# Kernel tuning notes

Measured on AMD Instinct MI355X. Metric: run time of the kernel, lower is better.

## Reference

```python
import jax, jax.numpy as jnp
import numpy as np

CHUNK = 64  # _HYMBA_SCAN_CHUNK default
HEAD_DIM = 128
STATE_DIM = 128


def setup_inputs() -> dict:
    key = jax.random.key(0)
    ks = jax.random.split(key, 6)
    B, T = 8, 8192
    x = jax.random.normal(ks[0], (B, T, HEAD_DIM), dtype=jnp.float32)
    log_A = jax.random.normal(ks[1], (STATE_DIM,), dtype=jnp.float32) * 0.5
    # torch Linear weights are (out_features, in_features); kaiming-uniform-ish init
    lim = 1.0 / np.sqrt(HEAD_DIM)
    W_B = jax.random.uniform(ks[2], (STATE_DIM, HEAD_DIM), jnp.float32, -lim, lim)
    W_C = jax.random.uniform(ks[3], (STATE_DIM, HEAD_DIM), jnp.float32, -lim, lim)
    W_dt = jax.random.uniform(ks[4], (STATE_DIM, HEAD_DIM), jnp.float32, -lim, lim)
    b_dt = jnp.full((STATE_DIM,), -4.0, dtype=jnp.float32)
    lim_o = 1.0 / np.sqrt(STATE_DIM)
    W_out = jax.random.uniform(ks[5], (HEAD_DIM, STATE_DIM), jnp.float32, -lim_o, lim_o)
    return {"x": x, "log_A": log_A, "W_B": W_B, "W_C": W_C,
            "W_dt": W_dt, "b_dt": b_dt, "W_out": W_out}


def _scan_chunks(log_a, u, chunk_size=CHUNK):
    # log_a, u: (B, T, S) fp32; exact chunk-parallel diagonal recurrence
    B, T, S = u.shape
    nc = T // chunk_size
    la = log_a.reshape(B, nc, chunk_size, S).transpose(1, 0, 2, 3)  # (nc,B,ck,S)
    uu = u.reshape(B, nc, chunk_size, S).transpose(1, 0, 2, 3)

    def step(h0, inp):
        la_c, u_c = inp                                   # (B, ck, S)
        log_p = jnp.clip(jnp.cumsum(la_c, axis=1), -30.0, 0.0)
        p = jnp.exp(log_p)
        h = p * jnp.cumsum(u_c * jnp.exp(-log_p), axis=1) + p * h0[:, None, :]
        return h[:, -1, :], h

    h0 = jnp.zeros((B, S), dtype=jnp.float32)
    _, h_chunks = jax.lax.scan(step, h0, (la, uu))        # (nc, B, ck, S)
    return h_chunks.transpose(1, 0, 2, 3).reshape(B, T, S)


def reference(x, log_A, W_B, W_C, W_dt, b_dt, W_out):
    xf = x.astype(jnp.float32)
    dt = jnp.minimum(jax.nn.softplus(jnp.einsum('btd,sd->bts', xf, W_dt) + b_dt), 1.0)
    A = -jnp.minimum(jnp.exp(log_A.astype(jnp.float32)), 10.0)   # (S,)
    log_a = jnp.clip(dt * A[None, None, :], -0.5, 0.0)
    Bx = jnp.einsum('btd,sd->bts', xf, W_B) * dt
    C = jnp.einsum('btd,sd->bts', xf, W_C)
    h = _scan_chunks(log_a, Bx)                                   # (B,T,S)
    y = jnp.sum(C * h, axis=-1, keepdims=True)                    # (B,T,1)
    out = jnp.einsum('bts,ds->btd', h.astype(x.dtype), W_out)
    return out + y.astype(x.dtype) * x[..., :1]
```

## Files before the change

### kernel.cpp

```cpp
#include <hip/hip_runtime.h>
#include <hip/hip_bf16.h>

#define B_ 8
#define T_ 8192
#define D_ 128
#define S_ 128
#define CK 64
#define NC 128
#define NCHUNK (B_*NC)

typedef __attribute__((ext_vector_type(8))) __bf16 bf16x8;
typedef __attribute__((ext_vector_type(4))) float floatx4;

#define WS_WBF     0
#define WS_AVEC    32768
#define WS_PART    32896

__device__ __forceinline__ unsigned short f2bf(float f) {
  __hip_bfloat16 b = __float2bfloat16(f);
  return *(unsigned short*)&b;
}

__device__ __forceinline__ float softplus1(float z) {
  float sp = fmaxf(z, 0.0f) + __logf(1.0f + __expf(-fabsf(z)));
  return fminf(sp, 1.0f);
}

__device__ __forceinline__ unsigned long long part_load(const unsigned long long* p) {
  return __hip_atomic_load(p, __ATOMIC_RELAXED, __HIP_MEMORY_SCOPE_AGENT);
}
__device__ __forceinline__ void part_store(unsigned long long* p, unsigned long long v) {
  __hip_atomic_store(p, v, __ATOMIC_RELAXED, __HIP_MEMORY_SCOPE_AGENT);
}

__global__ __launch_bounds__(256) void k0_prep(
    const float* __restrict__ Wdt, const float* __restrict__ WB,
    const float* __restrict__ WC,  const float* __restrict__ Wout,
    const float* __restrict__ logA, float* __restrict__ ws) {
  unsigned short* wb = (unsigned short*)(ws + WS_WBF);
  const float* srcs[4] = {Wdt, WB, WC, Wout};
  int gid = blockIdx.x * 256 + threadIdx.x;
#pragma unroll
  for (int r = 0; r < 2; ++r) {
    int fid = gid * 2 + r;
    int lane = fid & 63;
    int kk   = (fid >> 6) & 3;
    int nt   = (fid >> 8) & 7;
    int m    = fid >> 11;
    int c = lane & 15, g = lane >> 4;
    const float* src = srcs[m] + (16 * nt + c) * 128 + 32 * kk + 8 * g;
    float4 v0 = *(const float4*)src;
    float4 v1 = *(const float4*)(src + 4);
    unsigned short o[8];
    o[0] = f2bf(v0.x); o[1] = f2bf(v0.y); o[2] = f2bf(v0.z); o[3] = f2bf(v0.w);
    o[4] = f2bf(v1.x); o[5] = f2bf(v1.y); o[6] = f2bf(v1.z); o[7] = f2bf(v1.w);
    *(ushort4*)&wb[fid * 8]     = *(ushort4*)&o[0];
    *(ushort4*)&wb[fid * 8 + 4] = *(ushort4*)&o[4];
  }
  unsigned long long* part = (unsigned long long*)(ws + WS_PART);
#pragma unroll
  for (int i = 0; i < 32; ++i)
    part[gid + 4096 * i] = 0ull;
  if (blockIdx.x == 0 && threadIdx.x < 128)
    ws[WS_AVEC + threadIdx.x] = -fminf(expf(logA[threadIdx.x]), 10.0f);
}

#define WFRAG(mat, nt, kk) \
  (*(const bf16x8*)&wb[(((((mat) * 8 + (nt)) * 4) + (kk)) * 64 + lane) * 8])

__global__ __launch_bounds__(256, 2) void k_main(
    const float* __restrict__ x, const float* __restrict__ bdt,
    float* __restrict__ out, float* __restrict__ ws) {
  __shared__ __align__(16) unsigned short xb[64 * 136];
  __shared__ float wlsP[4 * 128];
  __shared__ float wlsH[4 * 128];
  __shared__ float h0buf[128];
  __shared__ float yx[64];

  const int tid  = threadIdx.x;
  const int bc   = blockIdx.x;
  const int b    = bc & 7;
  const int cidx = bc >> 3;
  const long chunk_t0 = (long)b * T_ + (long)cidx * CK;
  const int w    = tid >> 6;
  const int lane = tid & 63;
  const int g    = lane >> 4;
  const int c    = lane & 15;

  float Av[8], Bd[8];
#pragma unroll
  for (int nt = 0; nt < 8; ++nt) {
    Av[nt] = ws[WS_AVEC + 16 * nt + c];
    Bd[nt] = bdt[16 * nt + c];
  }
  float x0[4];
  if (c == 0) {
#pragma unroll
    for (int i = 0; i < 4; ++i)
      x0[i] = x[(chunk_t0 + 16 * w + 4 * g + i) * D_];
  }

  const float4* x4 = (const float4*)(x + chunk_t0 * D_);
#pragma unroll
  for (int i = 0; i < 8; ++i) {
    int f4 = tid + 256 * i;
    int t  = f4 >> 5;
    int d0 = (f4 & 31) << 2;
    float4 v = x4[f4];
    ushort4 o;
    o.x = f2bf(v.x); o.y = f2bf(v.y); o.z = f2bf(v.z); o.w = f2bf(v.w);
    *(ushort4*)&xb[t * 136 + d0] = o;
  }
  __syncthreads();

  bf16x8 afr[4];
#pragma unroll
  for (int kk = 0; kk < 4; ++kk)
    afr[kk] = *(const bf16x8*)&xb[(16 * w + c) * 136 + 8 * g + 32 * kk];

  const unsigned short* wb = (const unsigned short*)(ws + WS_WBF);
  unsigned long long* part = (unsigned long long*)(ws + WS_PART);

  floatx4 dtacc[8], bacc[8];
#pragma unroll
  for (int nt = 0; nt < 8; ++nt) {
    dtacc[nt] = (floatx4){0.f, 0.f, 0.f, 0.f};
    bacc[nt]  = (floatx4){0.f, 0.f, 0.f, 0.f};
  }

  {
    bf16x8 fD[8], fB[8];
#pragma unroll
    for (int nt = 0; nt < 8; ++nt) fD[nt] = WFRAG(0, nt, 0);
#pragma unroll
    for (int nt = 0; nt < 8; ++nt) fB[nt] = WFRAG(1, nt, 0);
#pragma unroll
    for (int kk = 0; kk < 4; ++kk) {
      bf16x8 nD[8], nB[8];
      if (kk < 3) {
#pragma unroll
        for (int nt = 0; nt < 8; ++nt) nD[nt] = WFRAG(0, nt, kk + 1);
#pragma unroll
        for (int nt = 0; nt < 8; ++nt) nB[nt] = WFRAG(1, nt, kk + 1);
      }
#pragma unroll
      for (int nt = 0; nt < 8; ++nt) {
        dtacc[nt] = __builtin_amdgcn_mfma_f32_16x16x32_bf16(afr[kk], fD[nt], dtacc[nt], 0, 0, 0);
        bacc[nt]  = __builtin_amdgcn_mfma_f32_16x16x32_bf16(afr[kk], fB[nt], bacc[nt], 0, 0, 0);
      }
      if (kk < 3) {
#pragma unroll
        for (int nt = 0; nt < 8; ++nt) { fD[nt] = nD[nt]; fB[nt] = nB[nt]; }
      }
    }
  }

#pragma unroll
  for (int nt = 0; nt < 8; ++nt)
#pragma unroll
    for (int i = 0; i < 4; ++i) {
      float dt = softplus1(dtacc[nt][i] + Bd[nt]);
      float u  = bacc[nt][i] * dt;
      float la = fmaxf(fminf(dt * Av[nt], 0.0f), -0.5f);
      dtacc[nt][i] = __expf(la);
      bacc[nt][i]  = u;
    }

#pragma unroll
  for (int nt = 0; nt < 8; ++nt) {
    float P = dtacc[nt][0], H = bacc[nt][0];
#pragma unroll
    for (int i = 1; i < 4; ++i) {
      H = fmaf(H, dtacc[nt][i], bacc[nt][i]);
      P = P * dtacc[nt][i];
      dtacc[nt][i] = P;
      bacc[nt][i]  = H;
    }
  }
#pragma unroll
  for (int nt = 0; nt < 8; ++nt) {
    float P = dtacc[nt][3], H = bacc[nt][3];
    float Po = __shfl(P, (lane - 16) & 63), Ho = __shfl(H, (lane - 16) & 63);
    if (g >= 1) { H = fmaf(Ho, P, H); P = Po * P; }
    Po = __shfl(P, (lane - 32) & 63); Ho = __shfl(H, (lane - 32) & 63);
    if (g >= 2) { H = fmaf(Ho, P, H); P = Po * P; }
    float Pe = __shfl(P, (lane - 16) & 63), He = __shfl(H, (lane - 16) & 63);
    if (g == 0) { Pe = 1.0f; He = 0.0f; }
#pragma unroll
    for (int i = 0; i < 4; ++i) {
      bacc[nt][i] = fmaf(dtacc[nt][i], He, bacc[nt][i]);
      dtacc[nt][i] = dtacc[nt][i] * Pe;
    }
    if (g == 3) {
      wlsP[w * 128 + 16 * nt + c] = dtacc[nt][3];
      wlsH[w * 128 + 16 * nt + c] = bacc[nt][3];
    }
  }
  __syncthreads();

  if (tid < 128) {
    float Pt = 1.0f, Ht = 0.0f;
#pragma unroll
    for (int ww = 0; ww < 4; ++ww) {
      float Pw = wlsP[ww * 128 + tid];
      float Hw = wlsH[ww * 128 + tid];
      Ht = fmaf(Ht, Pw, Hw);
      Pt = Pt * Pw;
    }
    unsigned long long v = ((unsigned long long)__float_as_uint(Ht) << 32) |
                           (unsigned long long)__float_as_uint(Pt);
    part_store(&part[bc * 128 + tid], v);
  }

#pragma unroll
  for (int nt = 0; nt < 8; ++nt) {
    float Pe = 1.0f, He = 0.0f;
    for (int ww = 0; ww < 3; ++ww) {
      if (ww < w) {
        float Pw = wlsP[ww * 128 + 16 * nt + c];
        float Hw = wlsH[ww * 128 + 16 * nt + c];
        He = fmaf(He, Pw, Hw);
        Pe = Pe * Pw;
      }
    }
#pragma unroll
    for (int i = 0; i < 4; ++i) {
      bacc[nt][i] = fmaf(dtacc[nt][i], He, bacc[nt][i]);
      dtacc[nt][i] = dtacc[nt][i] * Pe;
    }
  }

  floatx4 cacc[8];
#pragma unroll
  for (int nt = 0; nt < 8; ++nt) cacc[nt] = (floatx4){0.f, 0.f, 0.f, 0.f};
  {
    bf16x8 fC[8];
#pragma unroll
    for (int nt = 0; nt < 8; ++nt) fC[nt] = WFRAG(2, nt, 0);
#pragma unroll
    for (int kk = 0; kk < 4; ++kk) {
      bf16x8 nC[8];
      if (kk < 3) {
#pragma unroll
        for (int nt = 0; nt < 8; ++nt) nC[nt] = WFRAG(2, nt, kk + 1);
      }
#pragma unroll
      for (int nt = 0; nt < 8; ++nt)
        cacc[nt] = __builtin_amdgcn_mfma_f32_16x16x32_bf16(afr[kk], fC[nt], cacc[nt], 0, 0, 0);
      if (kk < 3) {
#pragma unroll
        for (int nt = 0; nt < 8; ++nt) fC[nt] = nC[nt];
      }
    }
  }

  __syncthreads();

  if (tid < 128) {
    float RP = 1.0f, RH = 0.0f;
    int j = cidx - 1;
    while (j >= 0) {
      int nb = (j >= 7) ? 8 : (j + 1);
      unsigned long long v[8];
#pragma unroll
      for (int q = 0; q < 8; ++q)
        if (q < nb) v[q] = part_load(&part[(((j - q) << 3) | b) * 128 + tid]);
#pragma unroll
      for (int q = 0; q < 8; ++q) {
        if (q < nb) {
          unsigned long long vv = v[q];
          const unsigned long long* ap = &part[(((j - q) << 3) | b) * 128 + tid];
          while ((unsigned)vv == 0u) {
            __builtin_amdgcn_s_sleep(2);
            vv = part_load(ap);
          }
          float Pj = __uint_as_float((unsigned)vv);
          float Hj = __uint_as_float((unsigned)(vv >> 32));
          RH = fmaf(RP, Hj, RH);
          RP = RP * Pj;
        }
      }
      j -= nb;
    }
    h0buf[tid] = RH;
  }
  __syncthreads();

  float h0[8];
#pragma unroll
  for (int nt = 0; nt < 8; ++nt) h0[nt] = h0buf[16 * nt + c];

  float yv[4] = {0.f, 0.f, 0.f, 0.f};
  unsigned short* hT = xb;
#pragma unroll
  for (int nt = 0; nt < 8; ++nt)
#pragma unroll
    for (int i = 0; i < 4; ++i) {
      float hv = fmaf(dtacc[nt][i], h0[nt], bacc[nt][i]);
      yv[i] = fmaf(cacc[nt][i], hv, yv[i]);
      hT[(16 * w + 4 * g + i) * 136 + 16 * nt + c] = f2bf(hv);
    }
#pragma unroll
  for (int i = 0; i < 4; ++i) {
    yv[i] += __shfl_xor(yv[i], 1);
    yv[i] += __shfl_xor(yv[i], 2);
    yv[i] += __shfl_xor(yv[i], 4);
    yv[i] += __shfl_xor(yv[i], 8);
  }
  if (c == 0) {
#pragma unroll
    for (int i = 0; i < 4; ++i) yx[16 * w + 4 * g + i] = yv[i] * x0[i];
  }

  bf16x8 fO[8];
#pragma unroll
  for (int nt = 0; nt < 8; ++nt) fO[nt] = WFRAG(3, nt, 0);
  __syncthreads();

  bf16x8 hfr[4];
#pragma unroll
  for (int kk = 0; kk < 4; ++kk)
    hfr[kk] = *(const bf16x8*)&hT[(16 * w + c) * 136 + 8 * g + 32 * kk];

  floatx4 oacc[8];
#pragma unroll
  for (int nt = 0; nt < 8; ++nt) oacc[nt] = (floatx4){0.f, 0.f, 0.f, 0.f};
#pragma unroll
  for (int kk = 0; kk < 4; ++kk) {
    bf16x8 nO[8];
    if (kk < 3) {
#pragma unroll
      for (int nt = 0; nt < 8; ++nt) nO[nt] = WFRAG(3, nt, kk + 1);
    }
#pragma unroll
    for (int nt = 0; nt < 8; ++nt)
      oacc[nt] = __builtin_amdgcn_mfma_f32_16x16x32_bf16(hfr[kk], fO[nt], oacc[nt], 0, 0, 0);
    if (kk < 3) {
#pragma unroll
      for (int nt = 0; nt < 8; ++nt) fO[nt] = nO[nt];
    }
  }

#pragma unroll
  for (int nt = 0; nt < 8; ++nt)
#pragma unroll
    for (int i = 0; i < 4; ++i) {
      int row = 16 * w + 4 * g + i;
      out[(chunk_t0 + row) * D_ + 16 * nt + c] = oacc[nt][i] + yx[row];
    }
}

extern "C" void kernel_launch(void* const* d_in, const int* in_sizes, int n_in,
                              void* d_out, int out_size, void* d_ws, size_t ws_size,
                              hipStream_t stream) {
  const float* x    = (const float*)d_in[0];
  const float* logA = (const float*)d_in[1];
  const float* W_B  = (const float*)d_in[2];
  const float* W_C  = (const float*)d_in[3];
  const float* W_dt = (const float*)d_in[4];
  const float* b_dt = (const float*)d_in[5];
  const float* W_out= (const float*)d_in[6];
  float* out = (float*)d_out;
  float* ws  = (float*)d_ws;

  k0_prep<<<16, 256, 0, stream>>>(W_dt, W_B, W_C, W_out, logA, ws);
  k_main<<<NCHUNK, 256, 0, stream>>>(x, b_dt, out, ws);
}
```

Measured before the change: 134.1 us.

## Repartition waves by state columns, split decoupled lookback across half-waves

The four waves now each own 32 state columns across all 64 timesteps, instead of 16 timesteps across all 128 columns. Each wave does the full intra-chunk scan on its own, so the LDS exchange of per-wave carries and one barrier go away, and each wave loads a quarter of the weight fragments. The cross-chunk lookback is split between the two halves of each wave, which walk disjoint ranges of previous chunks, and the results are combined with a shuffle. The y reduction across waves now goes through LDS, launch bounds allow 3 blocks per CU, and the prep kernel uses more blocks with less work per thread. In exchange, A fragments are re-read from LDS per M tile, which raises LDS traffic.

```diff
diff --git a/kernel.cpp b/kernel.cpp
--- a/kernel.cpp
+++ b/kernel.cpp
@@ -40,9 +40,8 @@
   unsigned short* wb = (unsigned short*)(ws + WS_WBF);
   const float* srcs[4] = {Wdt, WB, WC, Wout};
   int gid = blockIdx.x * 256 + threadIdx.x;
-#pragma unroll
-  for (int r = 0; r < 2; ++r) {
-    int fid = gid * 2 + r;
+  {
+    int fid = gid;
     int lane = fid & 63;
     int kk   = (fid >> 6) & 3;
     int nt   = (fid >> 8) & 7;
@@ -59,8 +58,8 @@
   }
   unsigned long long* part = (unsigned long long*)(ws + WS_PART);
 #pragma unroll
-  for (int i = 0; i < 32; ++i)
-    part[gid + 4096 * i] = 0ull;
+  for (int i = 0; i < 16; ++i)
+    part[gid + 8192 * i] = 0ull;
   if (blockIdx.x == 0 && threadIdx.x < 128)
     ws[WS_AVEC + threadIdx.x] = -fminf(expf(logA[threadIdx.x]), 10.0f);
 }
@@ -68,14 +67,12 @@
 #define WFRAG(mat, nt, kk) \
   (*(const bf16x8*)&wb[(((((mat) * 8 + (nt)) * 4) + (kk)) * 64 + lane) * 8])
 
-__global__ __launch_bounds__(256, 2) void k_main(
+__global__ __launch_bounds__(256, 3) void k_main(
     const float* __restrict__ x, const float* __restrict__ bdt,
     float* __restrict__ out, float* __restrict__ ws) {
   __shared__ __align__(16) unsigned short xb[64 * 136];
-  __shared__ float wlsP[4 * 128];
-  __shared__ float wlsH[4 * 128];
-  __shared__ float h0buf[128];
-  __shared__ float yx[64];
+  __shared__ float x0s[64];
+  __shared__ float yxa[4 * 64];
 
   const int tid  = threadIdx.x;
   const int bc   = blockIdx.x;
@@ -87,17 +84,12 @@
   const int g    = lane >> 4;
   const int c    = lane & 15;
 
-  float Av[8], Bd[8];
-#pragma unroll
-  for (int nt = 0; nt < 8; ++nt) {
-    Av[nt] = ws[WS_AVEC + 16 * nt + c];
-    Bd[nt] = bdt[16 * nt + c];
-  }
-  float x0[4];
-  if (c == 0) {
-#pragma unroll
-    for (int i = 0; i < 4; ++i)
-      x0[i] = x[(chunk_t0 + 16 * w + 4 * g + i) * D_];
+  float Av2[2], Bd2[2];
+#pragma unroll
+  for (int ntl = 0; ntl < 2; ++ntl) {
+    int s = 32 * w + 16 * ntl + c;
+    Av2[ntl] = ws[WS_AVEC + s];
+    Bd2[ntl] = bdt[s];
   }
 
   const float4* x4 = (const float4*)(x + chunk_t0 * D_);
@@ -111,165 +103,171 @@
     o.x = f2bf(v.x); o.y = f2bf(v.y); o.z = f2bf(v.z); o.w = f2bf(v.w);
     *(ushort4*)&xb[t * 136 + d0] = o;
   }
+  if (tid < 64) x0s[tid] = x[(chunk_t0 + tid) * D_];
   __syncthreads();
-
-  bf16x8 afr[4];
-#pragma unroll
-  for (int kk = 0; kk < 4; ++kk)
-    afr[kk] = *(const bf16x8*)&xb[(16 * w + c) * 136 + 8 * g + 32 * kk];
 
   const unsigned short* wb = (const unsigned short*)(ws + WS_WBF);
   unsigned long long* part = (unsigned long long*)(ws + WS_PART);
 
-  floatx4 dtacc[8], bacc[8];
-#pragma unroll
-  for (int nt = 0; nt < 8; ++nt) {
-    dtacc[nt] = (floatx4){0.f, 0.f, 0.f, 0.f};
-    bacc[nt]  = (floatx4){0.f, 0.f, 0.f, 0.f};
-  }
-
-  {
-    bf16x8 fD[8], fB[8];
-#pragma unroll
-    for (int nt = 0; nt < 8; ++nt) fD[nt] = WFRAG(0, nt, 0);
-#pragma unroll
-    for (int nt = 0; nt < 8; ++nt) fB[nt] = WFRAG(1, nt, 0);
+  floatx4 A_[2][4], U_[2][4];
+#pragma unroll
+  for (int ntl = 0; ntl < 2; ++ntl)
+#pragma unroll
+    for (int mt = 0; mt < 4; ++mt) {
+      A_[ntl][mt] = (floatx4){0.f, 0.f, 0.f, 0.f};
+      U_[ntl][mt] = (floatx4){0.f, 0.f, 0.f, 0.f};
+    }
+  {
+    bf16x8 a4[4], fD[2], fB[2];
+#pragma unroll
+    for (int mt = 0; mt < 4; ++mt)
+      a4[mt] = *(const bf16x8*)&xb[(16 * mt + c) * 136 + 8 * g];
+#pragma unroll
+    for (int ntl = 0; ntl < 2; ++ntl) {
+      fD[ntl] = WFRAG(0, 2 * w + ntl, 0);
+      fB[ntl] = WFRAG(1, 2 * w + ntl, 0);
+    }
 #pragma unroll
     for (int kk = 0; kk < 4; ++kk) {
-      bf16x8 nD[8], nB[8];
-      if (kk < 3) {
-#pragma unroll
-        for (int nt = 0; nt < 8; ++nt) nD[nt] = WFRAG(0, nt, kk + 1);
-#pragma unroll
-        for (int nt = 0; nt < 8; ++nt) nB[nt] = WFRAG(1, nt, kk + 1);
-      }
-#pragma unroll
-      for (int nt = 0; nt < 8; ++nt) {
-        dtacc[nt] = __builtin_amdgcn_mfma_f32_16x16x32_bf16(afr[kk], fD[nt], dtacc[nt], 0, 0, 0);
-        bacc[nt]  = __builtin_amdgcn_mfma_f32_16x16x32_bf16(afr[kk], fB[nt], bacc[nt], 0, 0, 0);
-      }
-      if (kk < 3) {
-#pragma unroll
-        for (int nt = 0; nt < 8; ++nt) { fD[nt] = nD[nt]; fB[nt] = nB[nt]; }
-      }
-    }
-  }
-
-#pragma unroll
-  for (int nt = 0; nt < 8; ++nt)
-#pragma unroll
-    for (int i = 0; i < 4; ++i) {
-      float dt = softplus1(dtacc[nt][i] + Bd[nt]);
-      float u  = bacc[nt][i] * dt;
-      float la = fmaxf(fminf(dt * Av[nt], 0.0f), -0.5f);
-      dtacc[nt][i] = __expf(la);
-      bacc[nt][i]  = u;
-    }
-
-#pragma unroll
-  for (int nt = 0; nt < 8; ++nt) {
-    float P = dtacc[nt][0], H = bacc[nt][0];
-#pragma unroll
-    for (int i = 1; i < 4; ++i) {
-      H = fmaf(H, dtacc[nt][i], bacc[nt][i]);
-      P = P * dtacc[nt][i];
-      dtacc[nt][i] = P;
-      bacc[nt][i]  = H;
-    }
-  }
-#pragma unroll
-  for (int nt = 0; nt < 8; ++nt) {
-    float P = dtacc[nt][3], H = bacc[nt][3];
-    float Po = __shfl(P, (lane - 16) & 63), Ho = __shfl(H, (lane - 16) & 63);
-    if (g >= 1) { H = fmaf(Ho, P, H); P = Po * P; }
-    Po = __shfl(P, (lane - 32) & 63); Ho = __shfl(H, (lane - 32) & 63);
-    if (g >= 2) { H = fmaf(Ho, P, H); P = Po * P; }
-    float Pe = __shfl(P, (lane - 16) & 63), He = __shfl(H, (lane - 16) & 63);
-    if (g == 0) { Pe = 1.0f; He = 0.0f; }
-#pragma unroll
-    for (int i = 0; i < 4; ++i) {
-      bacc[nt][i] = fmaf(dtacc[nt][i], He, bacc[nt][i]);
-      dtacc[nt][i] = dtacc[nt][i] * Pe;
-    }
-    if (g == 3) {
-      wlsP[w * 128 + 16 * nt + c] = dtacc[nt][3];
-      wlsH[w * 128 + 16 * nt + c] = bacc[nt][3];
-    }
-  }
-  __syncthreads();
-
-  if (tid < 128) {
-    float Pt = 1.0f, Ht = 0.0f;
-#pragma unroll
-    for (int ww = 0; ww < 4; ++ww) {
-      float Pw = wlsP[ww * 128 + tid];
-      float Hw = wlsH[ww * 128 + tid];
-      Ht = fmaf(Ht, Pw, Hw);
-      Pt = Pt * Pw;
-    }
-    unsigned long long v = ((unsigned long long)__float_as_uint(Ht) << 32) |
-                           (unsigned long long)__float_as_uint(Pt);
-    part_store(&part[bc * 128 + tid], v);
-  }
-
-#pragma unroll
-  for (int nt = 0; nt < 8; ++nt) {
-    float Pe = 1.0f, He = 0.0f;
-    for (int ww = 0; ww < 3; ++ww) {
-      if (ww < w) {
-        float Pw = wlsP[ww * 128 + 16 * nt + c];
-        float Hw = wlsH[ww * 128 + 16 * nt + c];
-        He = fmaf(He, Pw, Hw);
-        Pe = Pe * Pw;
-      }
-    }
-#pragma unroll
-    for (int i = 0; i < 4; ++i) {
-      bacc[nt][i] = fmaf(dtacc[nt][i], He, bacc[nt][i]);
-      dtacc[nt][i] = dtacc[nt][i] * Pe;
-    }
-  }
-
-  floatx4 cacc[8];
-#pragma unroll
-  for (int nt = 0; nt < 8; ++nt) cacc[nt] = (floatx4){0.f, 0.f, 0.f, 0.f};
-  {
-    bf16x8 fC[8];
-#pragma unroll
-    for (int nt = 0; nt < 8; ++nt) fC[nt] = WFRAG(2, nt, 0);
+      bf16x8 na4[4], nD[2], nB[2];
+      if (kk < 3) {
+#pragma unroll
+        for (int mt = 0; mt < 4; ++mt)
+          na4[mt] = *(const bf16x8*)&xb[(16 * mt + c) * 136 + 8 * g + 32 * (kk + 1)];
+#pragma unroll
+        for (int ntl = 0; ntl < 2; ++ntl) {
+          nD[ntl] = WFRAG(0, 2 * w + ntl, kk + 1);
+          nB[ntl] = WFRAG(1, 2 * w + ntl, kk + 1);
+        }
+      }
+#pragma unroll
+      for (int ntl = 0; ntl < 2; ++ntl)
+#pragma unroll
+        for (int mt = 0; mt < 4; ++mt) {
+          A_[ntl][mt] = __builtin_amdgcn_mfma_f32_16x16x32_bf16(a4[mt], fD[ntl], A_[ntl][mt], 0, 0, 0);
+          U_[ntl][mt] = __builtin_amdgcn_mfma_f32_16x16x32_bf16(a4[mt], fB[ntl], U_[ntl][mt], 0, 0, 0);
+        }
+      if (kk < 3) {
+#pragma unroll
+        for (int mt = 0; mt < 4; ++mt) a4[mt] = na4[mt];
+#pragma unroll
+        for (int ntl = 0; ntl < 2; ++ntl) { fD[ntl] = nD[ntl]; fB[ntl] = nB[ntl]; }
+      }
+    }
+  }
+
+#pragma unroll
+  for (int ntl = 0; ntl < 2; ++ntl)
+#pragma unroll
+    for (int mt = 0; mt < 4; ++mt)
+#pragma unroll
+      for (int i = 0; i < 4; ++i) {
+        float dt = softplus1(A_[ntl][mt][i] + Bd2[ntl]);
+        float u  = U_[ntl][mt][i] * dt;
+        float la = fmaxf(fminf(dt * Av2[ntl], 0.0f), -0.5f);
+        A_[ntl][mt][i] = __expf(la);
+        U_[ntl][mt][i] = u;
+      }
+
+  float PcT[2], HcT[2];
+#pragma unroll
+  for (int ntl = 0; ntl < 2; ++ntl) {
+    float Pc = 1.0f, Hc = 0.0f;
+#pragma unroll
+    for (int mt = 0; mt < 4; ++mt) {
+      float P = A_[ntl][mt][0], H = U_[ntl][mt][0];
+#pragma unroll
+      for (int i = 1; i < 4; ++i) {
+        H = fmaf(H, A_[ntl][mt][i], U_[ntl][mt][i]);
+        P = P * A_[ntl][mt][i];
+        A_[ntl][mt][i] = P;
+        U_[ntl][mt][i] = H;
+      }
+      float Po = __shfl(P, (lane - 16) & 63), Ho = __shfl(H, (lane - 16) & 63);
+      if (g >= 1) { H = fmaf(Ho, P, H); P = Po * P; }
+      Po = __shfl(P, (lane - 32) & 63); Ho = __shfl(H, (lane - 32) & 63);
+      if (g >= 2) { H = fmaf(Ho, P, H); P = Po * P; }
+      float Pt = __shfl(P, 48 + c);
+      float Ht = __shfl(H, 48 + c);
+      float Pe = __shfl(P, (lane - 16) & 63), He = __shfl(H, (lane - 16) & 63);
+      if (g == 0) { Pe = 1.0f; He = 0.0f; }
+      float Hent = fmaf(Pe, Hc, He);
+      float Pent = Pe * Pc;
+#pragma unroll
+      for (int i = 0; i < 4; ++i) {
+        U_[ntl][mt][i] = fmaf(A_[ntl][mt][i], Hent, U_[ntl][mt][i]);
+        A_[ntl][mt][i] = A_[ntl][mt][i] * Pent;
+      }
+      Hc = fmaf(Pt, Hc, Ht);
+      Pc = Pc * Pt;
+    }
+    PcT[ntl] = Pc; HcT[ntl] = Hc;
+  }
+
+  if (g == 0) {
+#pragma unroll
+    for (int ntl = 0; ntl < 2; ++ntl) {
+      unsigned long long v = ((unsigned long long)__float_as_uint(HcT[ntl]) << 32) |
+                             (unsigned long long)__float_as_uint(PcT[ntl]);
+      part_store(&part[bc * 128 + 32 * w + 16 * ntl + c], v);
+    }
+  }
+
+  floatx4 Cc[2][4];
+#pragma unroll
+  for (int ntl = 0; ntl < 2; ++ntl)
+#pragma unroll
+    for (int mt = 0; mt < 4; ++mt) Cc[ntl][mt] = (floatx4){0.f, 0.f, 0.f, 0.f};
+  {
+    bf16x8 a4[4], fC[2];
+#pragma unroll
+    for (int mt = 0; mt < 4; ++mt)
+      a4[mt] = *(const bf16x8*)&xb[(16 * mt + c) * 136 + 8 * g];
+#pragma unroll
+    for (int ntl = 0; ntl < 2; ++ntl) fC[ntl] = WFRAG(2, 2 * w + ntl, 0);
 #pragma unroll
     for (int kk = 0; kk < 4; ++kk) {
-      bf16x8 nC[8];
-      if (kk < 3) {
-#pragma unroll
-        for (int nt = 0; nt < 8; ++nt) nC[nt] = WFRAG(2, nt, kk + 1);
-      }
-#pragma unroll
-      for (int nt = 0; nt < 8; ++nt)
-        cacc[nt] = __builtin_amdgcn_mfma_f32_16x16x32_bf16(afr[kk], fC[nt], cacc[nt], 0, 0, 0);
-      if (kk < 3) {
-#pragma unroll
-        for (int nt = 0; nt < 8; ++nt) fC[nt] = nC[nt];
-      }
-    }
-  }
-
-  __syncthreads();
-
-  if (tid < 128) {
+      bf16x8 na4[4], nC[2];
+      if (kk < 3) {
+#pragma unroll
+        for (int mt = 0; mt < 4; ++mt)
+          na4[mt] = *(const bf16x8*)&xb[(16 * mt + c) * 136 + 8 * g + 32 * (kk + 1)];
+#pragma unroll
+        for (int ntl = 0; ntl < 2; ++ntl) nC[ntl] = WFRAG(2, 2 * w + ntl, kk + 1);
+      }
+#pragma unroll
+      for (int ntl = 0; ntl < 2; ++ntl)
+#pragma unroll
+        for (int mt = 0; mt < 4; ++mt)
+          Cc[ntl][mt] = __builtin_amdgcn_mfma_f32_16x16x32_bf16(a4[mt], fC[ntl], Cc[ntl][mt], 0, 0, 0);
+      if (kk < 3) {
+#pragma unroll
+        for (int mt = 0; mt < 4; ++mt) a4[mt] = na4[mt];
+#pragma unroll
+        for (int ntl = 0; ntl < 2; ++ntl) fC[ntl] = nC[ntl];
+      }
+    }
+  }
+
+  float h0v[2];
+  {
+    const int s    = 32 * w + (lane & 31);
+    const int half = lane >> 5;
     float RP = 1.0f, RH = 0.0f;
-    int j = cidx - 1;
-    while (j >= 0) {
-      int nb = (j >= 7) ? 8 : (j + 1);
+    const int K   = (cidx + 1) >> 1;
+    int j         = half ? (cidx - K - 1) : (cidx - 1);
+    const int jlo = half ? 0 : (cidx - K);
+    while (j >= jlo) {
+      int nb = j - jlo + 1; if (nb > 8) nb = 8;
       unsigned long long v[8];
 #pragma unroll
       for (int q = 0; q < 8; ++q)
-        if (q < nb) v[q] = part_load(&part[(((j - q) << 3) | b) * 128 + tid]);
+        if (q < nb) v[q] = part_load(&part[(((j - q) << 3) | b) * 128 + s]);
 #pragma unroll
       for (int q = 0; q < 8; ++q) {
         if (q < nb) {
           unsigned long long vv = v[q];
-          const unsigned long long* ap = &part[(((j - q) << 3) | b) * 128 + tid];
+          const unsigned long long* ap = &part[(((j - q) << 3) | b) * 128 + s];
           while ((unsigned)vv == 0u) {
             __builtin_amdgcn_s_sleep(2);
             vv = part_load(ap);
@@ -282,71 +280,98 @@
       }
       j -= nb;
     }
-    h0buf[tid] = RH;
-  }
+    float oP = __shfl_xor(RP, 32), oH = __shfl_xor(RH, 32);
+    float Pn = half ? oP : RP, Hn = half ? oH : RH;
+    float Hf = half ? RH : oH;
+    float H0 = fmaf(Pn, Hf, Hn);
+#pragma unroll
+    for (int ntl = 0; ntl < 2; ++ntl)
+      h0v[ntl] = __shfl(H0, 16 * ntl + c);
+  }
+
   __syncthreads();
 
-  float h0[8];
-#pragma unroll
-  for (int nt = 0; nt < 8; ++nt) h0[nt] = h0buf[16 * nt + c];
-
-  float yv[4] = {0.f, 0.f, 0.f, 0.f};
-  unsigned short* hT = xb;
-#pragma unroll
-  for (int nt = 0; nt < 8; ++nt)
+  float yv[4][4];
+#pragma unroll
+  for (int mt = 0; mt < 4; ++mt)
+#pragma unroll
+    for (int i = 0; i < 4; ++i) yv[mt][i] = 0.0f;
+#pragma unroll
+  for (int ntl = 0; ntl < 2; ++ntl)
+#pragma unroll
+    for (int mt = 0; mt < 4; ++mt)
+#pragma unroll
+      for (int i = 0; i < 4; ++i) {
+        float hv = fmaf(A_[ntl][mt][i], h0v[ntl], U_[ntl][mt][i]);
+        yv[mt][i] = fmaf(Cc[ntl][mt][i], hv, yv[mt][i]);
+        xb[(16 * mt + 4 * g + i) * 136 + 32 * w + 16 * ntl + c] = f2bf(hv);
+      }
+#pragma unroll
+  for (int mt = 0; mt < 4; ++mt)
 #pragma unroll
     for (int i = 0; i < 4; ++i) {
-      float hv = fmaf(dtacc[nt][i], h0[nt], bacc[nt][i]);
-      yv[i] = fmaf(cacc[nt][i], hv, yv[i]);
-      hT[(16 * w + 4 * g + i) * 136 + 16 * nt + c] = f2bf(hv);
-    }
-#pragma unroll
-  for (int i = 0; i < 4; ++i) {
-    yv[i] += __shfl_xor(yv[i], 1);
-    yv[i] += __shfl_xor(yv[i], 2);
-    yv[i] += __shfl_xor(yv[i], 4);
-    yv[i] += __shfl_xor(yv[i], 8);
-  }
-  if (c == 0) {
-#pragma unroll
-    for (int i = 0; i < 4; ++i) yx[16 * w + 4 * g + i] = yv[i] * x0[i];
-  }
-
-  bf16x8 fO[8];
-#pragma unroll
-  for (int nt = 0; nt < 8; ++nt) fO[nt] = WFRAG(3, nt, 0);
+      float y = yv[mt][i];
+      y += __shfl_xor(y, 1);
+      y += __shfl_xor(y, 2);
+      y += __shfl_xor(y, 4);
+      y += __shfl_xor(y, 8);
+      if (c == 0) yxa[w * 64 + 16 * mt + 4 * g + i] = y;
+    }
+
+  bf16x8 fO[2];
+#pragma unroll
+  for (int ntl = 0; ntl < 2; ++ntl) fO[ntl] = WFRAG(3, 2 * w + ntl, 0);
+
   __syncthreads();
-
-  bf16x8 hfr[4];
-#pragma unroll
-  for (int kk = 0; kk < 4; ++kk)
-    hfr[kk] = *(const bf16x8*)&hT[(16 * w + c) * 136 + 8 * g + 32 * kk];
-
-  floatx4 oacc[8];
-#pragma unroll
-  for (int nt = 0; nt < 8; ++nt) oacc[nt] = (floatx4){0.f, 0.f, 0.f, 0.f};
-#pragma unroll
-  for (int kk = 0; kk < 4; ++kk) {
-    bf16x8 nO[8];
-    if (kk < 3) {
-#pragma unroll
-      for (int nt = 0; nt < 8; ++nt) nO[nt] = WFRAG(3, nt, kk + 1);
-    }
-#pragma unroll
-    for (int nt = 0; nt < 8; ++nt)
-      oacc[nt] = __builtin_amdgcn_mfma_f32_16x16x32_bf16(hfr[kk], fO[nt], oacc[nt], 0, 0, 0);
-    if (kk < 3) {
-#pragma unroll
-      for (int nt = 0; nt < 8; ++nt) fO[nt] = nO[nt];
-    }
-  }
-
-#pragma unroll
-  for (int nt = 0; nt < 8; ++nt)
+  if (tid < 64) {
+    float y = yxa[tid] + yxa[64 + tid] + yxa[128 + tid] + yxa[192 + tid];
+    x0s[tid] = y * x0s[tid];
+  }
+  __syncthreads();
+
+  floatx4 Oc[2][4];
+#pragma unroll
+  for (int ntl = 0; ntl < 2; ++ntl)
+#pragma unroll
+    for (int mt = 0; mt < 4; ++mt) Oc[ntl][mt] = (floatx4){0.f, 0.f, 0.f, 0.f};
+  {
+    bf16x8 h4[4];
+#pragma unroll
+    for (int mt = 0; mt < 4; ++mt)
+      h4[mt] = *(const bf16x8*)&xb[(16 * mt + c) * 136 + 8 * g];
+#pragma unroll
+    for (int kk = 0; kk < 4; ++kk) {
+      bf16x8 nh4[4], nO[2];
+      if (kk < 3) {
+#pragma unroll
+        for (int mt = 0; mt < 4; ++mt)
+          nh4[mt] = *(const bf16x8*)&xb[(16 * mt + c) * 136 + 8 * g + 32 * (kk + 1)];
+#pragma unroll
+        for (int ntl = 0; ntl < 2; ++ntl) nO[ntl] = WFRAG(3, 2 * w + ntl, kk + 1);
+      }
+#pragma unroll
+      for (int ntl = 0; ntl < 2; ++ntl)
+#pragma unroll
+        for (int mt = 0; mt < 4; ++mt)
+          Oc[ntl][mt] = __builtin_amdgcn_mfma_f32_16x16x32_bf16(h4[mt], fO[ntl], Oc[ntl][mt], 0, 0, 0);
+      if (kk < 3) {
+#pragma unroll
+        for (int mt = 0; mt < 4; ++mt) h4[mt] = nh4[mt];
+#pragma unroll
+        for (int ntl = 0; ntl < 2; ++ntl) fO[ntl] = nO[ntl];
+      }
+    }
+  }
+
+#pragma unroll
+  for (int mt = 0; mt < 4; ++mt)
 #pragma unroll
     for (int i = 0; i < 4; ++i) {
-      int row = 16 * w + 4 * g + i;
-      out[(chunk_t0 + row) * D_ + 16 * nt + c] = oacc[nt][i] + yx[row];
+      int row = 16 * mt + 4 * g + i;
+      float yt = x0s[row];
+#pragma unroll
+      for (int ntl = 0; ntl < 2; ++ntl)
+        out[(chunk_t0 + row) * D_ + 32 * w + 16 * ntl + c] = Oc[ntl][mt][i] + yt;
     }
 }
 
@@ -363,6 +388,6 @@
   float* out = (float*)d_out;
   float* ws  = (float*)d_ws;
 
-  k0_prep<<<16, 256, 0, stream>>>(W_dt, W_B, W_C, W_out, logA, ws);
+  k0_prep<<<32, 256, 0, stream>>>(W_dt, W_B, W_C, W_out, logA, ws);
   k_main<<<NCHUNK, 256, 0, stream>>>(x, b_dt, out, ws);
 }
```

New measurement: 124.4 us. 1.08x faster.
